# Performance work log

Hardware: AMD Instinct MI355X
Metric: run time of the kernel (lower is better)

The kernel has to match this reference:

```python
import jax, jax.numpy as jnp
import numpy as np

N = 50000   # nnodes
E = 1600000 # edges (avg degree 32)
F = 128     # nfeatures
D = 64      # output_dim
T = 10      # s2v iterations (default in n2v)


def setup_inputs() -> dict:
    key = jax.random.key(0)
    k_x, k_s, k_d, k_w1, k_w2 = jax.random.split(key, 5)
    x = jax.random.normal(k_x, (N, F), dtype=jnp.float32)
    edge_src = jax.random.randint(k_s, (E,), 0, N, dtype=jnp.int32)
    edge_dst = jax.random.randint(k_d, (E,), 0, N, dtype=jnp.int32)
    # xavier_uniform init as in reset_parameters
    s1 = float(np.sqrt(6.0 / (F + D)))
    s2 = float(np.sqrt(6.0 / (D + D)))
    W1 = jax.random.uniform(k_w1, (D, F), jnp.float32, -s1, s1)
    W2 = jax.random.uniform(k_w2, (D, D), jnp.float32, -s2, s2)
    b1 = jnp.zeros((D,), jnp.float32)
    b2 = jnp.zeros((D,), jnp.float32)
    return {"x": x, "W1": W1, "b1": b1, "W2": W2, "b2": b2,
            "edge_src": edge_src, "edge_dst": edge_dst}


def reference(x, W1, b1, W2, b2, edge_src, edge_dst):
    Wx = x @ W1.T + b1                      # [N, D]

    def step(emb, _):
        # sum of neighbor embeddings: gather sources, segment-sum into dests
        agg = jax.ops.segment_sum(emb[edge_src], edge_dst, num_segments=N)  # [N, D]
        emb_new = jax.nn.relu(Wx + agg @ W2.T + b2)
        return emb_new, None

    emb0 = jnp.zeros((N, D), dtype=x.dtype)
    emb, _ = jax.lax.scan(step, emb0, None, length=T)  # n2v
    # g2v: sum node embeddings into graph embedding
    return emb.sum(axis=0)                  # [D]
```

## Files before the change

kernel.cpp:

```cpp
#include <hip/hip_runtime.h>

#define D 64
#define F 128
#define NBMAX 256

typedef unsigned int uint;
typedef unsigned short ushort;
typedef short s16x8 __attribute__((ext_vector_type(8)));
typedef float f32x4 __attribute__((ext_vector_type(4)));

__device__ __forceinline__ float bf16lo(uint u) { return __uint_as_float(u << 16); }
__device__ __forceinline__ float bf16hi(uint u) { return __uint_as_float(u & 0xFFFF0000u); }
__device__ __forceinline__ ushort f2bf16(float f) {
    uint u = __float_as_uint(f);
    u += 0x7FFFu + ((u >> 16) & 1u);
    return (ushort)(u >> 16);
}
__device__ __forceinline__ uint pk2bf(float lo, float hi) {
    return (uint)f2bf16(lo) | ((uint)f2bf16(hi) << 16);
}
__device__ __forceinline__ float rdlane(float v, int l) {
    return __uint_as_float(__builtin_amdgcn_readlane(__float_as_uint(v), l));
}


__global__ __launch_bounds__(256) void bucket_hist(const int* __restrict__ dst,
                                                   int* __restrict__ gb, int E, int nb) {
    __shared__ int h[NBMAX];
    for (int t = threadIdx.x; t < nb; t += 256) h[t] = 0;
    __syncthreads();
    int start = blockIdx.x * 4096;
    int end   = start + 4096 < E ? start + 4096 : E;
    for (int i = start + threadIdx.x; i < end; i += 256)
        atomicAdd(&h[dst[i] >> 8], 1);
    __syncthreads();
    for (int t = threadIdx.x; t < nb; t += 256)
        if (h[t]) atomicAdd(&gb[t], h[t]);
}

__global__ void bucket_scan(const int* __restrict__ gb, int* __restrict__ gboff,
                            int* __restrict__ gcur, int nb) {
    if (threadIdx.x == 0) {
        int s = 0;
        for (int b = 0; b < nb; ++b) { gboff[b] = s; gcur[b] = s; s += gb[b]; }
        gboff[nb] = s;
    }
}

__global__ __launch_bounds__(256) void bucket_scatter(const int* __restrict__ src,
                                                      const int* __restrict__ dst,
                                                      int* __restrict__ gcur,
                                                      int* __restrict__ packed, int E, int nb) {
    __shared__ int h[NBMAX], base[NBMAX], lcur[NBMAX];
    for (int t = threadIdx.x; t < nb; t += 256) h[t] = 0;
    __syncthreads();
    int start = blockIdx.x * 4096;
    int end   = start + 4096 < E ? start + 4096 : E;
    for (int i = start + threadIdx.x; i < end; i += 256)
        atomicAdd(&h[dst[i] >> 8], 1);
    __syncthreads();
    for (int t = threadIdx.x; t < nb; t += 256) {
        base[t] = h[t] ? atomicAdd(&gcur[t], h[t]) : 0;
        lcur[t] = 0;
    }
    __syncthreads();
    for (int i = start + threadIdx.x; i < end; i += 256) {
        int d = dst[i];
        int b = d >> 8;
        int pos = base[b] + atomicAdd(&lcur[b], 1);
        packed[pos] = (src[i] << 8) | (d & 255);
    }
}

__global__ __launch_bounds__(256) void bucket_deg(const int* __restrict__ gboff,
                                                  const int* __restrict__ packed,
                                                  int* __restrict__ deg, int N) {
    __shared__ int h[NBMAX];
    int b = blockIdx.x;
    h[threadIdx.x] = 0;
    __syncthreads();
    int st = gboff[b], en = gboff[b + 1];
    for (int i = st + threadIdx.x; i < en; i += 256)
        atomicAdd(&h[packed[i] & 255], 1);
    __syncthreads();
    int node = (b << 8) + threadIdx.x;
    if (node < N) deg[node] = h[threadIdx.x];
}

__global__ __launch_bounds__(256) void bucket_fill(const int* __restrict__ gboff,
                                                   const int* __restrict__ packed,
                                                   const int* __restrict__ row_ptr,
                                                   int* __restrict__ col, int N) {
    __shared__ int lcur[NBMAX];
    int b = blockIdx.x;
    int node = (b << 8) + threadIdx.x;
    lcur[threadIdx.x] = (node < N) ? row_ptr[node] : 0;
    __syncthreads();
    int st = gboff[b], en = gboff[b + 1];
    for (int i = st + threadIdx.x; i < en; i += 256) {
        int p = packed[i];
        int pos = atomicAdd(&lcur[p & 255], 1);
        col[pos] = p >> 8;
    }
}


__global__ void count_deg_kernel(const int* __restrict__ dst, int* __restrict__ deg, int E) {
    int i = blockIdx.x * blockDim.x + threadIdx.x;
    if (i < E) atomicAdd(&deg[dst[i]], 1);
}

__global__ void fill_kernel(const int* __restrict__ src, const int* __restrict__ dst,
                            int* __restrict__ cursor, int* __restrict__ col, int E) {
    int i = blockIdx.x * blockDim.x + threadIdx.x;
    if (i < E) {
        int d_ = dst[i];
        int pos = atomicAdd(&cursor[d_], 1);
        col[pos] = src[i];
    }
}


__global__ __launch_bounds__(1024) void scan_kernel(const int* __restrict__ deg,
                                                    int* __restrict__ row_ptr, int n) {
    __shared__ int wsum[16];
    int lane = threadIdx.x & 63;
    int wid  = threadIdx.x >> 6;
    int carry = 0;
    const int CH = 4096;
    for (int base = 0; base < n; base += CH) {
        int i0 = base + (int)threadIdx.x * 4;
        int v0 = (i0     < n) ? ((deg[i0]     + 15) & ~15) : 0;
        int v1 = (i0 + 1 < n) ? ((deg[i0 + 1] + 15) & ~15) : 0;
        int v2 = (i0 + 2 < n) ? ((deg[i0 + 2] + 15) & ~15) : 0;
        int v3 = (i0 + 3 < n) ? ((deg[i0 + 3] + 15) & ~15) : 0;
        int p0 = v0, p1 = p0 + v1, p2 = p1 + v2, p3 = p2 + v3;
        int tsum = p3;
        int s = tsum;
        #pragma unroll
        for (int off = 1; off < 64; off <<= 1) {
            int t = __shfl_up(s, off);
            if (lane >= off) s += t;
        }
        if (lane == 63) wsum[wid] = s;
        __syncthreads();
        int wbase = 0, chunk_total = 0;
        #pragma unroll
        for (int w = 0; w < 16; ++w) {
            int t = wsum[w];
            chunk_total += t;
            if (w < wid) wbase += t;
        }
        __syncthreads();
        int ex = carry + wbase + (s - tsum);
        if (i0     < n) row_ptr[i0 + 1] = ex + p0;
        if (i0 + 1 < n) row_ptr[i0 + 2] = ex + p1;
        if (i0 + 2 < n) row_ptr[i0 + 3] = ex + p2;
        if (i0 + 3 < n) row_ptr[i0 + 4] = ex + p3;
        carry += chunk_total;
    }
    if (threadIdx.x == 0) row_ptr[0] = 0;
}

__global__ void pad_kernel(const int* __restrict__ row_ptr, const int* __restrict__ deg,
                           int* __restrict__ col, int N) {
    int v = blockIdx.x * blockDim.x + threadIdx.x;
    if (v < N) {
        int st = row_ptr[v] + deg[v];
        int en = row_ptr[v + 1];
        for (int k = st; k < en; ++k) col[k] = N;
    }
}


__global__ __launch_bounds__(256) void wx_mfma_kernel(const float* __restrict__ x,
                                                      const float* __restrict__ W1,
                                                      const float* __restrict__ b1,
                                                      const float* __restrict__ b2,
                                                      float* __restrict__ Wx,
                                                      ushort* __restrict__ emb, int N) {
    int lane = threadIdx.x & 63;
    int wv = blockIdx.x * 4 + (threadIdx.x >> 6);
    int nwaves = gridDim.x * 4;
    int r16 = lane & 15;
    int kg  = lane >> 4;

    s16x8 bf[4][4];
    #pragma unroll
    for (int nt = 0; nt < 4; ++nt) {
        const float* wrow = W1 + (size_t)(nt * 16 + r16) * F;
        #pragma unroll
        for (int ks = 0; ks < 4; ++ks) {
            const float4* p = reinterpret_cast<const float4*>(wrow + ks * 32 + kg * 8);
            float4 f0 = p[0], f1 = p[1];
            union { s16x8 v; uint u[4]; } t;
            t.u[0] = pk2bf(f0.x, f0.y); t.u[1] = pk2bf(f0.z, f0.w);
            t.u[2] = pk2bf(f1.x, f1.y); t.u[3] = pk2bf(f1.z, f1.w);
            bf[nt][ks] = t.v;
        }
    }
    float b1v[4], b2v[4];
    #pragma unroll
    for (int nt = 0; nt < 4; ++nt) {
        b1v[nt] = b1[nt * 16 + r16];
        b2v[nt] = b2[nt * 16 + r16];
    }

    int ntiles = (N + 15) >> 4;
    for (int tile = wv; tile < ntiles; tile += nwaves) {
        int row0 = tile << 4;
        int arow = row0 + r16;
        if (arow >= N) arow = N - 1;
        s16x8 af[4];
        #pragma unroll
        for (int ks = 0; ks < 4; ++ks) {
            const float4* p = reinterpret_cast<const float4*>(x + (size_t)arow * F + ks * 32 + kg * 8);
            float4 f0 = p[0], f1 = p[1];
            union { s16x8 v; uint u[4]; } t;
            t.u[0] = pk2bf(f0.x, f0.y); t.u[1] = pk2bf(f0.z, f0.w);
            t.u[2] = pk2bf(f1.x, f1.y); t.u[3] = pk2bf(f1.z, f1.w);
            af[ks] = t.v;
        }
        #pragma unroll
        for (int nt = 0; nt < 4; ++nt) {
            f32x4 acc = {0.f, 0.f, 0.f, 0.f};
            #pragma unroll
            for (int ks = 0; ks < 4; ++ks)
                acc = __builtin_amdgcn_mfma_f32_16x16x32_bf16(af[ks], bf[nt][ks], acc, 0, 0, 0);
            int outd = nt * 16 + r16;
            #pragma unroll
            for (int r = 0; r < 4; ++r) {
                int node = row0 + kg * 4 + r;
                if (node < N) {
                    float wxv = acc[r] + b1v[nt];
                    Wx[(size_t)node * D + outd] = wxv;
                    float e = wxv + b2v[nt];
                    emb[(size_t)node * D + outd] = f2bf16(e > 0.f ? e : 0.f);
                }
            }
        }
    }
}


__global__ __launch_bounds__(256) void step_kernel(const ushort* __restrict__ emb_in,
                                                   ushort* __restrict__ emb_out,
                                                   const float* __restrict__ Wx,
                                                   const float* __restrict__ W2,
                                                   const float* __restrict__ b2,
                                                   const int* __restrict__ row_ptr,
                                                   const int* __restrict__ col, int N) {
    __shared__ float w2t[D][D + 1];
    int t = threadIdx.x;
    #pragma unroll
    for (int i = t; i < D * D; i += 256) {
        int dd = i >> 6, kk = i & 63;
        w2t[kk][dd] = W2[i];
    }
    __syncthreads();
    int lane = t & 63, wid = t >> 6;
    float b2v = b2[lane];
    int g = lane >> 3, s = lane & 7;
    int nw = gridDim.x * 4;
    for (int v = blockIdx.x * 4 + wid; v < N; v += nw) {
        int st = row_ptr[v], en = row_ptr[v + 1];
        float a0 = 0.f, a1 = 0.f, a2 = 0.f, a3 = 0.f, a4 = 0.f, a5 = 0.f, a6 = 0.f, a7 = 0.f;
        if (st < en) {
            int u0 = col[st + g], u1 = col[st + 8 + g];
            uint4 q0 = reinterpret_cast<const uint4*>(emb_in + ((size_t)u0 << 6))[s];
            uint4 q1 = reinterpret_cast<const uint4*>(emb_in + ((size_t)u1 << 6))[s];
            int k = st + 16;
            int n0 = N, n1 = N;
            if (k < en) { n0 = col[k + g]; n1 = col[k + 8 + g]; }
            for (; k < en; k += 16) {
                uint4 p0 = reinterpret_cast<const uint4*>(emb_in + ((size_t)n0 << 6))[s];
                uint4 p1 = reinterpret_cast<const uint4*>(emb_in + ((size_t)n1 << 6))[s];
                int k2 = k + 16;
                int m0 = N, m1 = N;
                if (k2 < en) { m0 = col[k2 + g]; m1 = col[k2 + 8 + g]; }
                a0 += bf16lo(q0.x); a1 += bf16hi(q0.x);
                a2 += bf16lo(q0.y); a3 += bf16hi(q0.y);
                a4 += bf16lo(q0.z); a5 += bf16hi(q0.z);
                a6 += bf16lo(q0.w); a7 += bf16hi(q0.w);
                a0 += bf16lo(q1.x); a1 += bf16hi(q1.x);
                a2 += bf16lo(q1.y); a3 += bf16hi(q1.y);
                a4 += bf16lo(q1.z); a5 += bf16hi(q1.z);
                a6 += bf16lo(q1.w); a7 += bf16hi(q1.w);
                q0 = p0; q1 = p1; n0 = m0; n1 = m1;
            }
            a0 += bf16lo(q0.x); a1 += bf16hi(q0.x);
            a2 += bf16lo(q0.y); a3 += bf16hi(q0.y);
            a4 += bf16lo(q0.z); a5 += bf16hi(q0.z);
            a6 += bf16lo(q0.w); a7 += bf16hi(q0.w);
            a0 += bf16lo(q1.x); a1 += bf16hi(q1.x);
            a2 += bf16lo(q1.y); a3 += bf16hi(q1.y);
            a4 += bf16lo(q1.z); a5 += bf16hi(q1.z);
            a6 += bf16lo(q1.w); a7 += bf16hi(q1.w);
        }
        #pragma unroll
        for (int off = 8; off < 64; off <<= 1) {
            a0 += __shfl_xor(a0, off); a1 += __shfl_xor(a1, off);
            a2 += __shfl_xor(a2, off); a3 += __shfl_xor(a3, off);
            a4 += __shfl_xor(a4, off); a5 += __shfl_xor(a5, off);
            a6 += __shfl_xor(a6, off); a7 += __shfl_xor(a7, off);
        }
        float r = Wx[(size_t)v * D + lane] + b2v;
        #pragma unroll
        for (int kk = 0; kk < D; ++kk) {
            float av;
            switch (kk & 7) {
                case 0: av = rdlane(a0, kk >> 3); break;
                case 1: av = rdlane(a1, kk >> 3); break;
                case 2: av = rdlane(a2, kk >> 3); break;
                case 3: av = rdlane(a3, kk >> 3); break;
                case 4: av = rdlane(a4, kk >> 3); break;
                case 5: av = rdlane(a5, kk >> 3); break;
                case 6: av = rdlane(a6, kk >> 3); break;
                default: av = rdlane(a7, kk >> 3); break;
            }
            r += av * w2t[kk][lane];
        }
        emb_out[(size_t)v * D + lane] = f2bf16(r > 0.f ? r : 0.f);
    }
}


__global__ __launch_bounds__(256) void reduce_kernel(const ushort* __restrict__ emb,
                                                     float* __restrict__ out, int N) {
    int lane = threadIdx.x & 63;
    int wid  = threadIdx.x >> 6;
    float acc = 0.f;
    int nw = gridDim.x * 4;
    for (int v = blockIdx.x * 4 + wid; v < N; v += nw)
        acc += __uint_as_float((uint)emb[(size_t)v * D + lane] << 16);
    __shared__ float red[256];
    red[threadIdx.x] = acc;
    __syncthreads();
    if (threadIdx.x < 64) {
        float sum = red[threadIdx.x] + red[threadIdx.x + 64] +
                    red[threadIdx.x + 128] + red[threadIdx.x + 192];
        atomicAdd(&out[threadIdx.x], sum);
    }
}

extern "C" void kernel_launch(void* const* d_in, const int* in_sizes, int n_in,
                              void* d_out, int out_size, void* d_ws, size_t ws_size,
                              hipStream_t stream) {
    const float* x    = (const float*)d_in[0];
    const float* W1   = (const float*)d_in[1];
    const float* b1   = (const float*)d_in[2];
    const float* W2   = (const float*)d_in[3];
    const float* b2   = (const float*)d_in[4];
    const int*   esrc = (const int*)d_in[5];
    const int*   edst = (const int*)d_in[6];
    int N = in_sizes[0] / F;
    int E = in_sizes[5];
    float* out = (float*)d_out;

    char* ws = (char*)d_ws;
    size_t off = 0;
    auto alloc = [&](size_t bytes) -> char* {
        char* p = ws + off;
        off += (bytes + 255) & ~(size_t)255;
        return p;
    };
    float*  Wx      = (float*)alloc((size_t)N * D * 4);
    ushort* embA    = (ushort*)alloc(((size_t)N + 1) * D * 2);
    ushort* embB    = (ushort*)alloc(((size_t)N + 1) * D * 2);
    int*    row_ptr = (int*)alloc(((size_t)N + 1) * 4);
    int*    deg     = (int*)alloc((size_t)N * 4);
    int*    col     = (int*)alloc(((size_t)E + 15 * (size_t)N) * 4);
    int*    packed  = (int*)alloc((size_t)E * 4);
    int*    gb      = (int*)alloc((NBMAX + 1) * 4);
    int*    gboff   = (int*)alloc((NBMAX + 1) * 4);
    int*    gcur    = (int*)alloc((NBMAX + 1) * 4);
    int*    cursor  = (int*)alloc((size_t)N * 4);

    hipMemsetAsync(out, 0, (size_t)out_size * 4, stream);
    hipMemsetAsync(embA + (size_t)N * D, 0, D * 2, stream);
    hipMemsetAsync(embB + (size_t)N * D, 0, D * 2, stream);

    int nb = ((N - 1) >> 8) + 1;
    int nchunks = (E + 4095) / 4096;
    if (N <= 65536) {
        hipMemsetAsync(gb, 0, (size_t)nb * 4, stream);
        bucket_hist<<<nchunks, 256, 0, stream>>>(edst, gb, E, nb);
        bucket_scan<<<1, 64, 0, stream>>>(gb, gboff, gcur, nb);
        bucket_scatter<<<nchunks, 256, 0, stream>>>(esrc, edst, gcur, packed, E, nb);
        bucket_deg<<<nb, 256, 0, stream>>>(gboff, packed, deg, N);
        scan_kernel<<<1, 1024, 0, stream>>>(deg, row_ptr, N);
        bucket_fill<<<nb, 256, 0, stream>>>(gboff, packed, row_ptr, col, N);
    } else {
        hipMemsetAsync(deg, 0, (size_t)N * 4, stream);
        count_deg_kernel<<<(E + 255) / 256, 256, 0, stream>>>(edst, deg, E);
        scan_kernel<<<1, 1024, 0, stream>>>(deg, row_ptr, N);
        hipMemcpyAsync(cursor, row_ptr, (size_t)N * 4, hipMemcpyDeviceToDevice, stream);
        fill_kernel<<<(E + 255) / 256, 256, 0, stream>>>(esrc, edst, cursor, col, E);
    }
    pad_kernel<<<(N + 255) / 256, 256, 0, stream>>>(row_ptr, deg, col, N);

    wx_mfma_kernel<<<256, 256, 0, stream>>>(x, W1, b1, b2, Wx, embA, N);

    ushort* pin = embA;
    ushort* pout = embB;
    for (int t = 1; t < 10; ++t) {
        step_kernel<<<2048, 256, 0, stream>>>(pin, pout, Wx, W2, b2, row_ptr, col, N);
        ushort* tmp = pin; pin = pout; pout = tmp;
    }
    reduce_kernel<<<256, 256, 0, stream>>>(pin, out, N);
}
```

Baseline: 526.8 us.

## Degree-sort nodes and compute step aggregation as per-row gather plus MFMA W2

Nodes are counting-sorted by degree into a permutation and renumbered. Each wave now handles a 16-node tile of similar degree: every lane gathers one node's neighbours sequentially, and the aggregate is multiplied by W2 with bf16 MFMA instead of a readlane and LDS scalar matvec. The 16-aligned CSR padding is removed, and Wx and emb are stored in permuted order so the gathers index renumbered rows. The cost is extra preprocessing kernels and per-lane strided neighbour loads, whose coalescing is worse than the previous per-node 8-lane gather. The aggregate is also rounded to bf16 before the matmul.

```diff
diff --git a/kernel.cpp b/kernel.cpp
--- a/kernel.cpp
+++ b/kernel.cpp
@@ -3,6 +3,7 @@
 #define D 64
 #define F 128
 #define NBMAX 256
+#define DB 128
 
 typedef unsigned int uint;
 typedef unsigned short ushort;
@@ -19,9 +20,6 @@
 __device__ __forceinline__ uint pk2bf(float lo, float hi) {
     return (uint)f2bf16(lo) | ((uint)f2bf16(hi) << 16);
 }
-__device__ __forceinline__ float rdlane(float v, int l) {
-    return __uint_as_float(__builtin_amdgcn_readlane(__float_as_uint(v), l));
-}
 
 
 __global__ __launch_bounds__(256) void bucket_hist(const int* __restrict__ dst,
@@ -90,6 +88,7 @@
 __global__ __launch_bounds__(256) void bucket_fill(const int* __restrict__ gboff,
                                                    const int* __restrict__ packed,
                                                    const int* __restrict__ row_ptr,
+                                                   const int* __restrict__ rank,
                                                    int* __restrict__ col, int N) {
     __shared__ int lcur[NBMAX];
     int b = blockIdx.x;
@@ -100,7 +99,7 @@
     for (int i = st + threadIdx.x; i < en; i += 256) {
         int p = packed[i];
         int pos = atomicAdd(&lcur[p & 255], 1);
-        col[pos] = p >> 8;
+        col[pos] = rank[p >> 8];
     }
 }
 
@@ -111,12 +110,64 @@
 }
 
 __global__ void fill_kernel(const int* __restrict__ src, const int* __restrict__ dst,
-                            int* __restrict__ cursor, int* __restrict__ col, int E) {
+                            int* __restrict__ cursor, const int* __restrict__ rank,
+                            int* __restrict__ col, int E) {
     int i = blockIdx.x * blockDim.x + threadIdx.x;
     if (i < E) {
         int d_ = dst[i];
         int pos = atomicAdd(&cursor[d_], 1);
-        col[pos] = src[i];
+        col[pos] = rank[src[i]];
+    }
+}
+
+
+__global__ __launch_bounds__(256) void dsort_hist(const int* __restrict__ deg,
+                                                  int* __restrict__ dh, int N) {
+    __shared__ int h[DB];
+    if (threadIdx.x < DB) h[threadIdx.x] = 0;
+    __syncthreads();
+    int start = blockIdx.x * 4096;
+    int end   = start + 4096 < N ? start + 4096 : N;
+    for (int i = start + threadIdx.x; i < end; i += 256) {
+        int d = deg[i];
+        atomicAdd(&h[d < DB - 1 ? d : DB - 1], 1);
+    }
+    __syncthreads();
+    if (threadIdx.x < DB && h[threadIdx.x]) atomicAdd(&dh[threadIdx.x], h[threadIdx.x]);
+}
+
+__global__ void dsort_scan(const int* __restrict__ dh, int* __restrict__ dcur) {
+    if (threadIdx.x == 0) {
+        int s = 0;
+        for (int b = 0; b < DB; ++b) { dcur[b] = s; s += dh[b]; }
+    }
+}
+
+__global__ __launch_bounds__(256) void dsort_scatter(const int* __restrict__ deg,
+                                                     int* __restrict__ dcur,
+                                                     int* __restrict__ perm,
+                                                     int* __restrict__ rank, int N) {
+    __shared__ int h[DB], base[DB], lc[DB];
+    if (threadIdx.x < DB) h[threadIdx.x] = 0;
+    __syncthreads();
+    int start = blockIdx.x * 4096;
+    int end   = start + 4096 < N ? start + 4096 : N;
+    for (int i = start + threadIdx.x; i < end; i += 256) {
+        int d = deg[i];
+        atomicAdd(&h[d < DB - 1 ? d : DB - 1], 1);
+    }
+    __syncthreads();
+    if (threadIdx.x < DB) {
+        base[threadIdx.x] = h[threadIdx.x] ? atomicAdd(&dcur[threadIdx.x], h[threadIdx.x]) : 0;
+        lc[threadIdx.x] = 0;
+    }
+    __syncthreads();
+    for (int i = start + threadIdx.x; i < end; i += 256) {
+        int d = deg[i];
+        int b = d < DB - 1 ? d : DB - 1;
+        int pos = base[b] + atomicAdd(&lc[b], 1);
+        perm[pos] = i;
+        rank[i] = pos;
     }
 }
 
@@ -130,10 +181,10 @@
     const int CH = 4096;
     for (int base = 0; base < n; base += CH) {
         int i0 = base + (int)threadIdx.x * 4;
-        int v0 = (i0     < n) ? ((deg[i0]     + 15) & ~15) : 0;
-        int v1 = (i0 + 1 < n) ? ((deg[i0 + 1] + 15) & ~15) : 0;
-        int v2 = (i0 + 2 < n) ? ((deg[i0 + 2] + 15) & ~15) : 0;
-        int v3 = (i0 + 3 < n) ? ((deg[i0 + 3] + 15) & ~15) : 0;
+        int v0 = (i0     < n) ? deg[i0]     : 0;
+        int v1 = (i0 + 1 < n) ? deg[i0 + 1] : 0;
+        int v2 = (i0 + 2 < n) ? deg[i0 + 2] : 0;
+        int v3 = (i0 + 3 < n) ? deg[i0 + 3] : 0;
         int p0 = v0, p1 = p0 + v1, p2 = p1 + v2, p3 = p2 + v3;
         int tsum = p3;
         int s = tsum;
@@ -162,21 +213,12 @@
     if (threadIdx.x == 0) row_ptr[0] = 0;
 }
 
-__global__ void pad_kernel(const int* __restrict__ row_ptr, const int* __restrict__ deg,
-                           int* __restrict__ col, int N) {
-    int v = blockIdx.x * blockDim.x + threadIdx.x;
-    if (v < N) {
-        int st = row_ptr[v] + deg[v];
-        int en = row_ptr[v + 1];
-        for (int k = st; k < en; ++k) col[k] = N;
-    }
-}
-
 
 __global__ __launch_bounds__(256) void wx_mfma_kernel(const float* __restrict__ x,
                                                       const float* __restrict__ W1,
                                                       const float* __restrict__ b1,
                                                       const float* __restrict__ b2,
+                                                      const int* __restrict__ perm,
                                                       float* __restrict__ Wx,
                                                       ushort* __restrict__ emb, int N) {
     int lane = threadIdx.x & 63;
@@ -211,10 +253,11 @@
         int row0 = tile << 4;
         int arow = row0 + r16;
         if (arow >= N) arow = N - 1;
+        int orig = perm[arow];
         s16x8 af[4];
         #pragma unroll
         for (int ks = 0; ks < 4; ++ks) {
-            const float4* p = reinterpret_cast<const float4*>(x + (size_t)arow * F + ks * 32 + kg * 8);
+            const float4* p = reinterpret_cast<const float4*>(x + (size_t)orig * F + ks * 32 + kg * 8);
             float4 f0 = p[0], f1 = p[1];
             union { s16x8 v; uint u[4]; } t;
             t.u[0] = pk2bf(f0.x, f0.y); t.u[1] = pk2bf(f0.z, f0.w);
@@ -249,78 +292,108 @@
                                                    const float* __restrict__ W2,
                                                    const float* __restrict__ b2,
                                                    const int* __restrict__ row_ptr,
-                                                   const int* __restrict__ col, int N) {
-    __shared__ float w2t[D][D + 1];
-    int t = threadIdx.x;
+                                                   const int* __restrict__ col,
+                                                   const int* __restrict__ perm, int N) {
+    int lane = threadIdx.x & 63;
+    int w = threadIdx.x >> 6;
+    int r = lane & 15;
+    int a = lane >> 4;
+
+    s16x8 af[4][2];
     #pragma unroll
-    for (int i = t; i < D * D; i += 256) {
-        int dd = i >> 6, kk = i & 63;
-        w2t[kk][dd] = W2[i];
-    }
-    __syncthreads();
-    int lane = t & 63, wid = t >> 6;
-    float b2v = b2[lane];
-    int g = lane >> 3, s = lane & 7;
-    int nw = gridDim.x * 4;
-    for (int v = blockIdx.x * 4 + wid; v < N; v += nw) {
-        int st = row_ptr[v], en = row_ptr[v + 1];
-        float a0 = 0.f, a1 = 0.f, a2 = 0.f, a3 = 0.f, a4 = 0.f, a5 = 0.f, a6 = 0.f, a7 = 0.f;
-        if (st < en) {
-            int u0 = col[st + g], u1 = col[st + 8 + g];
-            uint4 q0 = reinterpret_cast<const uint4*>(emb_in + ((size_t)u0 << 6))[s];
-            uint4 q1 = reinterpret_cast<const uint4*>(emb_in + ((size_t)u1 << 6))[s];
-            int k = st + 16;
-            int n0 = N, n1 = N;
-            if (k < en) { n0 = col[k + g]; n1 = col[k + 8 + g]; }
-            for (; k < en; k += 16) {
-                uint4 p0 = reinterpret_cast<const uint4*>(emb_in + ((size_t)n0 << 6))[s];
-                uint4 p1 = reinterpret_cast<const uint4*>(emb_in + ((size_t)n1 << 6))[s];
-                int k2 = k + 16;
-                int m0 = N, m1 = N;
-                if (k2 < en) { m0 = col[k2 + g]; m1 = col[k2 + 8 + g]; }
-                a0 += bf16lo(q0.x); a1 += bf16hi(q0.x);
-                a2 += bf16lo(q0.y); a3 += bf16hi(q0.y);
-                a4 += bf16lo(q0.z); a5 += bf16hi(q0.z);
-                a6 += bf16lo(q0.w); a7 += bf16hi(q0.w);
-                a0 += bf16lo(q1.x); a1 += bf16hi(q1.x);
-                a2 += bf16lo(q1.y); a3 += bf16hi(q1.y);
-                a4 += bf16lo(q1.z); a5 += bf16hi(q1.z);
-                a6 += bf16lo(q1.w); a7 += bf16hi(q1.w);
-                q0 = p0; q1 = p1; n0 = m0; n1 = m1;
-            }
-            a0 += bf16lo(q0.x); a1 += bf16hi(q0.x);
-            a2 += bf16lo(q0.y); a3 += bf16hi(q0.y);
-            a4 += bf16lo(q0.z); a5 += bf16hi(q0.z);
-            a6 += bf16lo(q0.w); a7 += bf16hi(q0.w);
-            a0 += bf16lo(q1.x); a1 += bf16hi(q1.x);
-            a2 += bf16lo(q1.y); a3 += bf16hi(q1.y);
-            a4 += bf16lo(q1.z); a5 += bf16hi(q1.z);
-            a6 += bf16lo(q1.w); a7 += bf16hi(q1.w);
-        }
-        #pragma unroll
-        for (int off = 8; off < 64; off <<= 1) {
-            a0 += __shfl_xor(a0, off); a1 += __shfl_xor(a1, off);
-            a2 += __shfl_xor(a2, off); a3 += __shfl_xor(a3, off);
-            a4 += __shfl_xor(a4, off); a5 += __shfl_xor(a5, off);
-            a6 += __shfl_xor(a6, off); a7 += __shfl_xor(a7, off);
-        }
-        float r = Wx[(size_t)v * D + lane] + b2v;
-        #pragma unroll
-        for (int kk = 0; kk < D; ++kk) {
-            float av;
-            switch (kk & 7) {
-                case 0: av = rdlane(a0, kk >> 3); break;
-                case 1: av = rdlane(a1, kk >> 3); break;
-                case 2: av = rdlane(a2, kk >> 3); break;
-                case 3: av = rdlane(a3, kk >> 3); break;
-                case 4: av = rdlane(a4, kk >> 3); break;
-                case 5: av = rdlane(a5, kk >> 3); break;
-                case 6: av = rdlane(a6, kk >> 3); break;
-                default: av = rdlane(a7, kk >> 3); break;
-            }
-            r += av * w2t[kk][lane];
-        }
-        emb_out[(size_t)v * D + lane] = f2bf16(r > 0.f ? r : 0.f);
+    for (int t = 0; t < 4; ++t)
+        #pragma unroll
+        for (int f = 0; f < 2; ++f) {
+            const float4* p = reinterpret_cast<const float4*>(W2 + (size_t)(t * 16 + r) * D + f * 32 + a * 8);
+            float4 f0 = p[0], f1 = p[1];
+            union { s16x8 v; uint u[4]; } tt;
+            tt.u[0] = pk2bf(f0.x, f0.y); tt.u[1] = pk2bf(f0.z, f0.w);
+            tt.u[2] = pk2bf(f1.x, f1.y); tt.u[3] = pk2bf(f1.z, f1.w);
+            af[t][f] = tt.v;
+        }
+    float4 b2v[4];
+    #pragma unroll
+    for (int t = 0; t < 4; ++t)
+        b2v[t] = *reinterpret_cast<const float4*>(b2 + t * 16 + a * 4);
+
+    int ntiles = (N + 15) >> 4;
+    int tile = blockIdx.x * 4 + w;
+    if (tile >= ntiles) return;
+
+    int rg = tile * 16 + r;
+    int rgc = rg < N ? rg : N - 1;
+    int node = perm[rgc];
+    int rp = row_ptr[node];
+    int degr = row_ptr[node + 1] - rp;
+    if (rg >= N) degr = 0;
+    int maxd = degr;
+    #pragma unroll
+    for (int off = 1; off < 16; off <<= 1) {
+        int o = __shfl_xor(maxd, off);
+        maxd = o > maxd ? o : maxd;
+    }
+
+    float acc0[8] = {0.f, 0.f, 0.f, 0.f, 0.f, 0.f, 0.f, 0.f};
+    float acc1[8] = {0.f, 0.f, 0.f, 0.f, 0.f, 0.f, 0.f, 0.f};
+
+    if (maxd > 0) {
+        int u0 = (0 < degr) ? col[rp] : N;
+        int u1 = (1 < degr) ? col[rp + 1] : N;
+        uint4 q00 = *reinterpret_cast<const uint4*>(emb_in + ((size_t)u0 << 6) + (a << 3));
+        uint4 q01 = *reinterpret_cast<const uint4*>(emb_in + ((size_t)u0 << 6) + 32 + (a << 3));
+        uint4 q10 = *reinterpret_cast<const uint4*>(emb_in + ((size_t)u1 << 6) + (a << 3));
+        uint4 q11 = *reinterpret_cast<const uint4*>(emb_in + ((size_t)u1 << 6) + 32 + (a << 3));
+        for (int k = 0; k < maxd; ++k) {
+            int un = (k + 2 < degr) ? col[rp + k + 2] : N;
+            uint4 p0 = *reinterpret_cast<const uint4*>(emb_in + ((size_t)un << 6) + (a << 3));
+            uint4 p1 = *reinterpret_cast<const uint4*>(emb_in + ((size_t)un << 6) + 32 + (a << 3));
+            acc0[0] += bf16lo(q00.x); acc0[1] += bf16hi(q00.x);
+            acc0[2] += bf16lo(q00.y); acc0[3] += bf16hi(q00.y);
+            acc0[4] += bf16lo(q00.z); acc0[5] += bf16hi(q00.z);
+            acc0[6] += bf16lo(q00.w); acc0[7] += bf16hi(q00.w);
+            acc1[0] += bf16lo(q01.x); acc1[1] += bf16hi(q01.x);
+            acc1[2] += bf16lo(q01.y); acc1[3] += bf16hi(q01.y);
+            acc1[4] += bf16lo(q01.z); acc1[5] += bf16hi(q01.z);
+            acc1[6] += bf16lo(q01.w); acc1[7] += bf16hi(q01.w);
+            q00 = q10; q01 = q11; q10 = p0; q11 = p1;
+        }
+    }
+
+    union { s16x8 v; uint u[4]; } B0, B1;
+    B0.u[0] = pk2bf(acc0[0], acc0[1]); B0.u[1] = pk2bf(acc0[2], acc0[3]);
+    B0.u[2] = pk2bf(acc0[4], acc0[5]); B0.u[3] = pk2bf(acc0[6], acc0[7]);
+    B1.u[0] = pk2bf(acc1[0], acc1[1]); B1.u[1] = pk2bf(acc1[2], acc1[3]);
+    B1.u[2] = pk2bf(acc1[4], acc1[5]); B1.u[3] = pk2bf(acc1[6], acc1[7]);
+
+    f32x4 d0 = {0.f, 0.f, 0.f, 0.f}, d1 = {0.f, 0.f, 0.f, 0.f};
+    f32x4 d2 = {0.f, 0.f, 0.f, 0.f}, d3 = {0.f, 0.f, 0.f, 0.f};
+    d0 = __builtin_amdgcn_mfma_f32_16x16x32_bf16(af[0][0], B0.v, d0, 0, 0, 0);
+    d1 = __builtin_amdgcn_mfma_f32_16x16x32_bf16(af[1][0], B0.v, d1, 0, 0, 0);
+    d2 = __builtin_amdgcn_mfma_f32_16x16x32_bf16(af[2][0], B0.v, d2, 0, 0, 0);
+    d3 = __builtin_amdgcn_mfma_f32_16x16x32_bf16(af[3][0], B0.v, d3, 0, 0, 0);
+    d0 = __builtin_amdgcn_mfma_f32_16x16x32_bf16(af[0][1], B1.v, d0, 0, 0, 0);
+    d1 = __builtin_amdgcn_mfma_f32_16x16x32_bf16(af[1][1], B1.v, d1, 0, 0, 0);
+    d2 = __builtin_amdgcn_mfma_f32_16x16x32_bf16(af[2][1], B1.v, d2, 0, 0, 0);
+    d3 = __builtin_amdgcn_mfma_f32_16x16x32_bf16(af[3][1], B1.v, d3, 0, 0, 0);
+
+    if (rg < N) {
+        const float* wxp = Wx + ((size_t)rg << 6);
+        ushort* op = emb_out + ((size_t)rg << 6);
+        #pragma unroll
+        for (int t = 0; t < 4; ++t) {
+            float4 wx4 = *reinterpret_cast<const float4*>(wxp + t * 16 + a * 4);
+            f32x4 dd = (t == 0) ? d0 : (t == 1) ? d1 : (t == 2) ? d2 : d3;
+            float e0 = wx4.x + b2v[t].x + dd[0];
+            float e1 = wx4.y + b2v[t].y + dd[1];
+            float e2 = wx4.z + b2v[t].z + dd[2];
+            float e3 = wx4.w + b2v[t].w + dd[3];
+            e0 = e0 > 0.f ? e0 : 0.f; e1 = e1 > 0.f ? e1 : 0.f;
+            e2 = e2 > 0.f ? e2 : 0.f; e3 = e3 > 0.f ? e3 : 0.f;
+            uint2 st;
+            st.x = pk2bf(e0, e1);
+            st.y = pk2bf(e2, e3);
+            *reinterpret_cast<uint2*>(op + t * 16 + a * 4) = st;
+        }
     }
 }
 
@@ -369,42 +442,55 @@
     ushort* embB    = (ushort*)alloc(((size_t)N + 1) * D * 2);
     int*    row_ptr = (int*)alloc(((size_t)N + 1) * 4);
     int*    deg     = (int*)alloc((size_t)N * 4);
-    int*    col     = (int*)alloc(((size_t)E + 15 * (size_t)N) * 4);
+    int*    col     = (int*)alloc((size_t)E * 4);
     int*    packed  = (int*)alloc((size_t)E * 4);
+    int*    perm    = (int*)alloc(((size_t)N + 16) * 4);
+    int*    rank    = (int*)alloc((size_t)N * 4);
     int*    gb      = (int*)alloc((NBMAX + 1) * 4);
     int*    gboff   = (int*)alloc((NBMAX + 1) * 4);
     int*    gcur    = (int*)alloc((NBMAX + 1) * 4);
+    int*    dh      = (int*)alloc(DB * 4);
+    int*    dcur    = (int*)alloc(DB * 4);
     int*    cursor  = (int*)alloc((size_t)N * 4);
 
     hipMemsetAsync(out, 0, (size_t)out_size * 4, stream);
     hipMemsetAsync(embA + (size_t)N * D, 0, D * 2, stream);
     hipMemsetAsync(embB + (size_t)N * D, 0, D * 2, stream);
+    hipMemsetAsync(dh, 0, DB * 4, stream);
 
     int nb = ((N - 1) >> 8) + 1;
-    int nchunks = (E + 4095) / 4096;
+    int nchunksE = (E + 4095) / 4096;
+    int nchunksN = (N + 4095) / 4096;
     if (N <= 65536) {
         hipMemsetAsync(gb, 0, (size_t)nb * 4, stream);
-        bucket_hist<<<nchunks, 256, 0, stream>>>(edst, gb, E, nb);
+        bucket_hist<<<nchunksE, 256, 0, stream>>>(edst, gb, E, nb);
         bucket_scan<<<1, 64, 0, stream>>>(gb, gboff, gcur, nb);
-        bucket_scatter<<<nchunks, 256, 0, stream>>>(esrc, edst, gcur, packed, E, nb);
+        bucket_scatter<<<nchunksE, 256, 0, stream>>>(esrc, edst, gcur, packed, E, nb);
         bucket_deg<<<nb, 256, 0, stream>>>(gboff, packed, deg, N);
+        dsort_hist<<<nchunksN, 256, 0, stream>>>(deg, dh, N);
+        dsort_scan<<<1, 64, 0, stream>>>(dh, dcur);
+        dsort_scatter<<<nchunksN, 256, 0, stream>>>(deg, dcur, perm, rank, N);
         scan_kernel<<<1, 1024, 0, stream>>>(deg, row_ptr, N);
-        bucket_fill<<<nb, 256, 0, stream>>>(gboff, packed, row_ptr, col, N);
+        bucket_fill<<<nb, 256, 0, stream>>>(gboff, packed, row_ptr, rank, col, N);
     } else {
         hipMemsetAsync(deg, 0, (size_t)N * 4, stream);
         count_deg_kernel<<<(E + 255) / 256, 256, 0, stream>>>(edst, deg, E);
+        dsort_hist<<<nchunksN, 256, 0, stream>>>(deg, dh, N);
+        dsort_scan<<<1, 64, 0, stream>>>(dh, dcur);
+        dsort_scatter<<<nchunksN, 256, 0, stream>>>(deg, dcur, perm, rank, N);
         scan_kernel<<<1, 1024, 0, stream>>>(deg, row_ptr, N);
         hipMemcpyAsync(cursor, row_ptr, (size_t)N * 4, hipMemcpyDeviceToDevice, stream);
-        fill_kernel<<<(E + 255) / 256, 256, 0, stream>>>(esrc, edst, cursor, col, E);
-    }
-    pad_kernel<<<(N + 255) / 256, 256, 0, stream>>>(row_ptr, deg, col, N);
-
-    wx_mfma_kernel<<<256, 256, 0, stream>>>(x, W1, b1, b2, Wx, embA, N);
-
+        fill_kernel<<<(E + 255) / 256, 256, 0, stream>>>(esrc, edst, cursor, rank, col, E);
+    }
+
+    wx_mfma_kernel<<<256, 256, 0, stream>>>(x, W1, b1, b2, perm, Wx, embA, N);
+
+    int ntiles = (N + 15) >> 4;
+    int sblocks = (ntiles + 3) / 4;
     ushort* pin = embA;
     ushort* pout = embB;
     for (int t = 1; t < 10; ++t) {
-        step_kernel<<<2048, 256, 0, stream>>>(pin, pout, Wx, W2, b2, row_ptr, col, N);
+        step_kernel<<<sblocks, 256, 0, stream>>>(pin, pout, Wx, W2, b2, row_ptr, col, perm, N);
         ushort* tmp = pin; pin = pout; pout = tmp;
     }
     reduce_kernel<<<256, 256, 0, stream>>>(pin, out, N);
```

Result: slower. 657.7 us (+24.9%).

## Fuse all propagation steps and final reduction into one persistent kernel with grid barrier

Applied to the files above, without the earlier changes.

Replaces the nine step launches and the reduce launch with a single persistent kernel that loops over iterations and synchronises blocks through an atomic-counter grid barrier. The grid size is taken from the occupancy query so that all blocks can be resident at once. The aim is to remove per-launch overhead and the kernel-boundary drains between steps. The cost is a spin barrier per iteration and a deadlock risk if not every block is co-resident, since the kernel is launched normally rather than cooperatively. It also hardcodes 256 CUs when sizing the grid.

```diff
diff --git a/kernel.cpp b/kernel.cpp
--- a/kernel.cpp
+++ b/kernel.cpp
@@ -243,16 +243,18 @@
 }
 
 
-__global__ __launch_bounds__(256) void step_kernel(const ushort* __restrict__ emb_in,
-                                                   ushort* __restrict__ emb_out,
-                                                   const float* __restrict__ Wx,
-                                                   const float* __restrict__ W2,
-                                                   const float* __restrict__ b2,
-                                                   const int* __restrict__ row_ptr,
-                                                   const int* __restrict__ col, int N) {
+__global__ __launch_bounds__(256) void steps_coop_kernel(ushort* __restrict__ embA,
+                                                         ushort* __restrict__ embB,
+                                                         const float* __restrict__ Wx,
+                                                         const float* __restrict__ W2,
+                                                         const float* __restrict__ b2,
+                                                         const int* __restrict__ row_ptr,
+                                                         const int* __restrict__ col,
+                                                         float* __restrict__ out,
+                                                         int* __restrict__ bar, int N) {
     __shared__ float w2t[D][D + 1];
+    __shared__ float red[256];
     int t = threadIdx.x;
-    #pragma unroll
     for (int i = t; i < D * D; i += 256) {
         int dd = i >> 6, kk = i & 63;
         w2t[kk][dd] = W2[i];
@@ -261,23 +263,38 @@
     int lane = t & 63, wid = t >> 6;
     float b2v = b2[lane];
     int g = lane >> 3, s = lane & 7;
-    int nw = gridDim.x * 4;
-    for (int v = blockIdx.x * 4 + wid; v < N; v += nw) {
-        int st = row_ptr[v], en = row_ptr[v + 1];
-        float a0 = 0.f, a1 = 0.f, a2 = 0.f, a3 = 0.f, a4 = 0.f, a5 = 0.f, a6 = 0.f, a7 = 0.f;
-        if (st < en) {
-            int u0 = col[st + g], u1 = col[st + 8 + g];
-            uint4 q0 = reinterpret_cast<const uint4*>(emb_in + ((size_t)u0 << 6))[s];
-            uint4 q1 = reinterpret_cast<const uint4*>(emb_in + ((size_t)u1 << 6))[s];
-            int k = st + 16;
-            int n0 = N, n1 = N;
-            if (k < en) { n0 = col[k + g]; n1 = col[k + 8 + g]; }
-            for (; k < en; k += 16) {
-                uint4 p0 = reinterpret_cast<const uint4*>(emb_in + ((size_t)n0 << 6))[s];
-                uint4 p1 = reinterpret_cast<const uint4*>(emb_in + ((size_t)n1 << 6))[s];
-                int k2 = k + 16;
-                int m0 = N, m1 = N;
-                if (k2 < en) { m0 = col[k2 + g]; m1 = col[k2 + 8 + g]; }
+    int nw = (int)gridDim.x * 4;
+    int nblocks = (int)gridDim.x;
+
+    ushort* pin = embA;
+    ushort* pout = embB;
+    for (int it = 1; it < 10; ++it) {
+        for (int v = (int)blockIdx.x * 4 + wid; v < N; v += nw) {
+            int st = row_ptr[v], en = row_ptr[v + 1];
+            float a0 = 0.f, a1 = 0.f, a2 = 0.f, a3 = 0.f, a4 = 0.f, a5 = 0.f, a6 = 0.f, a7 = 0.f;
+            if (st < en) {
+                int u0 = col[st + g], u1 = col[st + 8 + g];
+                uint4 q0 = reinterpret_cast<const uint4*>(pin + ((size_t)u0 << 6))[s];
+                uint4 q1 = reinterpret_cast<const uint4*>(pin + ((size_t)u1 << 6))[s];
+                int k = st + 16;
+                int n0 = N, n1 = N;
+                if (k < en) { n0 = col[k + g]; n1 = col[k + 8 + g]; }
+                for (; k < en; k += 16) {
+                    uint4 p0 = reinterpret_cast<const uint4*>(pin + ((size_t)n0 << 6))[s];
+                    uint4 p1 = reinterpret_cast<const uint4*>(pin + ((size_t)n1 << 6))[s];
+                    int k2 = k + 16;
+                    int m0 = N, m1 = N;
+                    if (k2 < en) { m0 = col[k2 + g]; m1 = col[k2 + 8 + g]; }
+                    a0 += bf16lo(q0.x); a1 += bf16hi(q0.x);
+                    a2 += bf16lo(q0.y); a3 += bf16hi(q0.y);
+                    a4 += bf16lo(q0.z); a5 += bf16hi(q0.z);
+                    a6 += bf16lo(q0.w); a7 += bf16hi(q0.w);
+                    a0 += bf16lo(q1.x); a1 += bf16hi(q1.x);
+                    a2 += bf16lo(q1.y); a3 += bf16hi(q1.y);
+                    a4 += bf16lo(q1.z); a5 += bf16hi(q1.z);
+                    a6 += bf16lo(q1.w); a7 += bf16hi(q1.w);
+                    q0 = p0; q1 = p1; n0 = m0; n1 = m1;
+                }
                 a0 += bf16lo(q0.x); a1 += bf16hi(q0.x);
                 a2 += bf16lo(q0.y); a3 += bf16hi(q0.y);
                 a4 += bf16lo(q0.z); a5 += bf16hi(q0.z);
@@ -286,60 +303,53 @@
                 a2 += bf16lo(q1.y); a3 += bf16hi(q1.y);
                 a4 += bf16lo(q1.z); a5 += bf16hi(q1.z);
                 a6 += bf16lo(q1.w); a7 += bf16hi(q1.w);
-                q0 = p0; q1 = p1; n0 = m0; n1 = m1;
             }
-            a0 += bf16lo(q0.x); a1 += bf16hi(q0.x);
-            a2 += bf16lo(q0.y); a3 += bf16hi(q0.y);
-            a4 += bf16lo(q0.z); a5 += bf16hi(q0.z);
-            a6 += bf16lo(q0.w); a7 += bf16hi(q0.w);
-            a0 += bf16lo(q1.x); a1 += bf16hi(q1.x);
-            a2 += bf16lo(q1.y); a3 += bf16hi(q1.y);
-            a4 += bf16lo(q1.z); a5 += bf16hi(q1.z);
-            a6 += bf16lo(q1.w); a7 += bf16hi(q1.w);
-        }
-        #pragma unroll
-        for (int off = 8; off < 64; off <<= 1) {
-            a0 += __shfl_xor(a0, off); a1 += __shfl_xor(a1, off);
-            a2 += __shfl_xor(a2, off); a3 += __shfl_xor(a3, off);
-            a4 += __shfl_xor(a4, off); a5 += __shfl_xor(a5, off);
-            a6 += __shfl_xor(a6, off); a7 += __shfl_xor(a7, off);
-        }
-        float r = Wx[(size_t)v * D + lane] + b2v;
-        #pragma unroll
-        for (int kk = 0; kk < D; ++kk) {
-            float av;
-            switch (kk & 7) {
-                case 0: av = rdlane(a0, kk >> 3); break;
-                case 1: av = rdlane(a1, kk >> 3); break;
-                case 2: av = rdlane(a2, kk >> 3); break;
-                case 3: av = rdlane(a3, kk >> 3); break;
-                case 4: av = rdlane(a4, kk >> 3); break;
-                case 5: av = rdlane(a5, kk >> 3); break;
-                case 6: av = rdlane(a6, kk >> 3); break;
-                default: av = rdlane(a7, kk >> 3); break;
+            #pragma unroll
+            for (int off = 8; off < 64; off <<= 1) {
+                a0 += __shfl_xor(a0, off); a1 += __shfl_xor(a1, off);
+                a2 += __shfl_xor(a2, off); a3 += __shfl_xor(a3, off);
+                a4 += __shfl_xor(a4, off); a5 += __shfl_xor(a5, off);
+                a6 += __shfl_xor(a6, off); a7 += __shfl_xor(a7, off);
             }
-            r += av * w2t[kk][lane];
-        }
-        emb_out[(size_t)v * D + lane] = f2bf16(r > 0.f ? r : 0.f);
-    }
-}
-
-
-__global__ __launch_bounds__(256) void reduce_kernel(const ushort* __restrict__ emb,
-                                                     float* __restrict__ out, int N) {
-    int lane = threadIdx.x & 63;
-    int wid  = threadIdx.x >> 6;
+            float r = Wx[(size_t)v * D + lane] + b2v;
+            #pragma unroll
+            for (int kk = 0; kk < D; ++kk) {
+                float av;
+                switch (kk & 7) {
+                    case 0: av = rdlane(a0, kk >> 3); break;
+                    case 1: av = rdlane(a1, kk >> 3); break;
+                    case 2: av = rdlane(a2, kk >> 3); break;
+                    case 3: av = rdlane(a3, kk >> 3); break;
+                    case 4: av = rdlane(a4, kk >> 3); break;
+                    case 5: av = rdlane(a5, kk >> 3); break;
+                    case 6: av = rdlane(a6, kk >> 3); break;
+                    default: av = rdlane(a7, kk >> 3); break;
+                }
+                r += av * w2t[kk][lane];
+            }
+            pout[(size_t)v * D + lane] = f2bf16(r > 0.f ? r : 0.f);
+        }
+        __syncthreads();
+        __threadfence();
+        if (t == 0) {
+            atomicAdd(bar, 1);
+            int target = it * nblocks;
+            while (__hip_atomic_load(bar, __ATOMIC_ACQUIRE, __HIP_MEMORY_SCOPE_AGENT) < target)
+                __builtin_amdgcn_s_sleep(2);
+        }
+        __syncthreads();
+        __threadfence();
+        ushort* tmp = pin; pin = pout; pout = tmp;
+    }
+
     float acc = 0.f;
-    int nw = gridDim.x * 4;
-    for (int v = blockIdx.x * 4 + wid; v < N; v += nw)
-        acc += __uint_as_float((uint)emb[(size_t)v * D + lane] << 16);
-    __shared__ float red[256];
-    red[threadIdx.x] = acc;
-    __syncthreads();
-    if (threadIdx.x < 64) {
-        float sum = red[threadIdx.x] + red[threadIdx.x + 64] +
-                    red[threadIdx.x + 128] + red[threadIdx.x + 192];
-        atomicAdd(&out[threadIdx.x], sum);
+    for (int v = (int)blockIdx.x * 4 + wid; v < N; v += nw)
+        acc += __uint_as_float((uint)pin[(size_t)v * D + lane] << 16);
+    red[t] = acc;
+    __syncthreads();
+    if (t < 64) {
+        float sum = red[t] + red[t + 64] + red[t + 128] + red[t + 192];
+        atomicAdd(&out[t], sum);
     }
 }
 
@@ -374,11 +384,13 @@
     int*    gb      = (int*)alloc((NBMAX + 1) * 4);
     int*    gboff   = (int*)alloc((NBMAX + 1) * 4);
     int*    gcur    = (int*)alloc((NBMAX + 1) * 4);
+    int*    bar     = (int*)alloc(256);
     int*    cursor  = (int*)alloc((size_t)N * 4);
 
     hipMemsetAsync(out, 0, (size_t)out_size * 4, stream);
     hipMemsetAsync(embA + (size_t)N * D, 0, D * 2, stream);
     hipMemsetAsync(embB + (size_t)N * D, 0, D * 2, stream);
+    hipMemsetAsync(bar, 0, 4, stream);
 
     int nb = ((N - 1) >> 8) + 1;
     int nchunks = (E + 4095) / 4096;
@@ -401,11 +413,14 @@
 
     wx_mfma_kernel<<<256, 256, 0, stream>>>(x, W1, b1, b2, Wx, embA, N);
 
-    ushort* pin = embA;
-    ushort* pout = embB;
-    for (int t = 1; t < 10; ++t) {
-        step_kernel<<<2048, 256, 0, stream>>>(pin, pout, Wx, W2, b2, row_ptr, col, N);
-        ushort* tmp = pin; pin = pout; pout = tmp;
-    }
-    reduce_kernel<<<256, 256, 0, stream>>>(pin, out, N);
-}
+    int maxb = 0;
+    if (hipOccupancyMaxActiveBlocksPerMultiprocessor(&maxb, steps_coop_kernel, 256, 0)
+            != hipSuccess || maxb <= 0)
+        maxb = 4;
+    if (maxb > 8) maxb = 8;
+    int grid = maxb * 256;
+    if (grid > 2048) grid = 2048;
+
+    steps_coop_kernel<<<grid, 256, 0, stream>>>(embA, embB, Wx, W2, b2, row_ptr, col,
+                                                out, bar, N);
+}
```

Measured after the change: 1.521 ms. 189% more time.
